# Kernel tuning notes

Hardware: AMD Instinct MI355X
Metric: run time of the kernel (lower is better)

The kernel has to match this reference:

```python
import jax, jax.numpy as jnp
import numpy as np

BN_EPS = 1e-5
INTERP_EPS = 1e-8


def _bn_relu(x, g, b, m, v):
    # eval-mode BatchNorm1d over channel dim (last axis here) + ReLU
    return jax.nn.relu((x - m) * (g / jnp.sqrt(v + BN_EPS)) + b)


def setup_inputs() -> dict:
    key = jax.random.key(0)
    ks = jax.random.split(key, 12)
    B, N, S, C1, C2 = 4, 16384, 1024, 128, 256
    Cin = C1 + C2  # 384
    H1, H2 = 256, 128
    inp = {
        "xyz1": jax.random.normal(ks[0], (B, N, 3), jnp.float32),
        "xyz2": jax.random.normal(ks[1], (B, S, 3), jnp.float32),
        "points1": jax.random.normal(ks[2], (B, N, C1), jnp.float32),
        "points2": jax.random.normal(ks[3], (B, S, C2), jnp.float32),
        # Conv1d(k=1, bias=False) weights: (out_ch, in_ch)
        "w1": jax.random.normal(ks[4], (H1, Cin), jnp.float32) * (1.0 / np.sqrt(Cin)),
        "g1": jax.random.uniform(ks[5], (H1,), jnp.float32, 0.5, 1.5),
        "b1": jax.random.normal(ks[6], (H1,), jnp.float32) * 0.1,
        "m1": jax.random.normal(ks[7], (H1,), jnp.float32) * 0.1,
        "v1": jax.random.uniform(ks[8], (H1,), jnp.float32, 0.5, 1.5),
        "w2": jax.random.normal(ks[9], (H2, H1), jnp.float32) * (1.0 / np.sqrt(H1)),
        "g2": jax.random.uniform(ks[10], (H2,), jnp.float32, 0.5, 1.5),
        "b2": jax.random.normal(ks[11], (H2,), jnp.float32) * 0.1,
        "m2": jnp.zeros((H2,), jnp.float32),
        "v2": jnp.ones((H2,), jnp.float32),
    }
    return inp


def reference(xyz1, xyz2, points1, points2, w1, g1, b1, m1, v1, w2, g2, b2, m2, v2):
    B, N, _ = xyz1.shape
    S = xyz2.shape[1]
    # squared pairwise distances (B, N, S) via ||a||^2 + ||b||^2 - 2 a.b
    sq = (
        jnp.sum(xyz1 * xyz1, -1)[:, :, None]
        + jnp.sum(xyz2 * xyz2, -1)[:, None, :]
        - 2.0 * jnp.einsum("bnd,bsd->bns", xyz1, xyz2)
    )
    neg_d, idx = jax.lax.top_k(-sq, 3)  # 3 nearest neighbors
    dists = -neg_d  # (B, N, 3) squared distances, ascending
    recip = 1.0 / (dists + INTERP_EPS)
    weight = recip / jnp.sum(recip, -1, keepdims=True)  # (B, N, 3)
    # gather neighbor features: (B, N, 3, C2)
    gathered = points2[jnp.arange(B)[:, None, None], idx]
    interpolated = jnp.einsum("bnk,bnkc->bnc", weight, gathered)
    new_points = jnp.concatenate([points1, interpolated], axis=-1)  # (B, N, Cin)
    h = _bn_relu(jnp.einsum("bnc,dc->bnd", new_points, w1), g1, b1, m1, v1)
    out = _bn_relu(jnp.einsum("bnc,dc->bnd", h, w2), g2, b2, m2, v2)
    return out
```

## Files before the change

kernel.cpp:

```cpp
#include <hip/hip_runtime.h>
#include <math.h>

#define B_    4
#define N_    16384
#define S_    1024
#define C1_   128
#define C2_   256
#define CIN_  384
#define H1_   256
#define H2_   128
#define BN_EPS_     1e-5f
#define INTERP_EPS_ 1e-8f

typedef _Float16 f16;
typedef _Float16 f16x4 __attribute__((ext_vector_type(4)));
typedef _Float16 f16x8 __attribute__((ext_vector_type(8)));
typedef float    f32x4 __attribute__((ext_vector_type(4)));

#define GLD16(g, l) \
  __builtin_amdgcn_global_load_lds((const __attribute__((address_space(1))) void*)(g), \
                                   (__attribute__((address_space(3))) void*)(l), 16, 0, 0)

#define WS_IDX 0
#define WS_W   786432
#define WS_H   1572864
#define WS_W1F 35127296
#define WS_W2F 35323904
#define WS_SC1 35389440
#define WS_SH1 35390464
#define WS_SC2 35391488
#define WS_SH2 35392000

__global__ __launch_bounds__(256) void prep_kernel(
    const float* __restrict__ w1, const float* __restrict__ w2,
    const float* __restrict__ g1, const float* __restrict__ b1,
    const float* __restrict__ m1, const float* __restrict__ v1,
    const float* __restrict__ g2, const float* __restrict__ b2,
    const float* __restrict__ m2, const float* __restrict__ v2,
    f16* __restrict__ w1f, f16* __restrict__ w2f,
    float* __restrict__ sc1, float* __restrict__ sh1,
    float* __restrict__ sc2, float* __restrict__ sh2)
{
    const int t = blockIdx.x * 256 + threadIdx.x;
    if (t < 98304) {
        w1f[t] = (f16)w1[t];
    } else if (t < 131072) {
        w2f[t - 98304] = (f16)w2[t - 98304];
    } else if (t < 131328) {
        const int c = t - 131072;
        const float s = g1[c] / sqrtf(v1[c] + BN_EPS_);
        sc1[c] = s; sh1[c] = b1[c] - m1[c] * s;
    } else if (t < 131456) {
        const int c = t - 131328;
        const float s = g2[c] / sqrtf(v2[c] + BN_EPS_);
        sc2[c] = s; sh2[c] = b2[c] - m2[c] * s;
    }
}

#define LESS_(e, ei, dj, ij) ((e) < (dj) || ((e) == (dj) && (ei) < (ij)))
#define INSERT_LEX(e, ei) do { \
    if (LESS_(e, ei, d[3], id[3])) { \
      if (LESS_(e, ei, d[2], id[2])) { d[3] = d[2]; id[3] = id[2]; \
        if (LESS_(e, ei, d[1], id[1])) { d[2] = d[1]; id[2] = id[1]; \
          if (LESS_(e, ei, d[0], id[0])) { d[1] = d[0]; id[1] = id[0]; d[0] = e; id[0] = ei; } \
          else { d[1] = e; id[1] = ei; } } \
        else { d[2] = e; id[2] = ei; } } \
      else { d[3] = e; id[3] = ei; } } } while (0)
#define CSWAP(a_, b_) do { \
    if (rd[b_] < rd[a_] || (rd[b_] == rd[a_] && ri[b_] < ri[a_])) { \
      double td = rd[a_]; rd[a_] = rd[b_]; rd[b_] = td; \
      int ti = ri[a_]; ri[a_] = ri[b_]; ri[b_] = ti; } } while (0)

__device__ __forceinline__ int qaddr(int s) { return s * 4 + (s >> 8) * 4; }

__global__ __launch_bounds__(256) void topk_kernel(
    const float* __restrict__ xyz1, const float* __restrict__ xyz2,
    int* __restrict__ idx_out, float* __restrict__ w_out)
{
    __shared__ float q[4128];
    const int b     = blockIdx.x >> 8;
    const int pbase = (blockIdx.x & 255) << 6;
    const int t     = threadIdx.x;

    for (int i = t; i < S_; i += 256) {
        const float* s = &xyz2[((size_t)b * S_ + i) * 3];
        const int a = qaddr(i);
        q[a] = s[0]; q[a + 1] = s[1]; q[a + 2] = s[2];
    }
    __syncthreads();

    const int p     = pbase + (t >> 2);
    const int chunk = t & 3;
    const float* pp = &xyz1[((size_t)b * N_ + p) * 3];
    const float px = pp[0], py = pp[1], pz = pp[2];

    float d[4] = {1e30f, 1e30f, 1e30f, 1e30f};
    int  id[4] = {0, 0, 0, 0};

    const int s0 = chunk << 8;
    for (int s = s0; s < s0 + 256; ++s) {
        const int a = qaddr(s);
        const float dx = px - q[a], dy = py - q[a + 1], dz = pz - q[a + 2];
        const float dd = fmaf(dx, dx, fmaf(dy, dy, dz * dz));
        if (dd < d[3]) {
            if (dd < d[2]) { d[3] = d[2]; id[3] = id[2];
                if (dd < d[1]) { d[2] = d[1]; id[2] = id[1];
                    if (dd < d[0]) { d[1] = d[0]; id[1] = id[0]; d[0] = dd; id[0] = s; }
                    else { d[1] = dd; id[1] = s; } }
                else { d[2] = dd; id[2] = s; } }
            else { d[3] = dd; id[3] = s; }
        }
    }

    #pragma unroll
    for (int msk = 1; msk <= 2; msk <<= 1) {
        float e0 = __shfl_xor(d[0], msk), e1 = __shfl_xor(d[1], msk);
        float e2 = __shfl_xor(d[2], msk), e3 = __shfl_xor(d[3], msk);
        int   j0 = __shfl_xor(id[0], msk), j1 = __shfl_xor(id[1], msk);
        int   j2 = __shfl_xor(id[2], msk), j3 = __shfl_xor(id[3], msk);
        INSERT_LEX(e0, j0); INSERT_LEX(e1, j1); INSERT_LEX(e2, j2); INSERT_LEX(e3, j3);
    }

    if (chunk == 0) {
        const double px6 = px, py6 = py, pz6 = pz;
        double rd[4]; int ri[4];
        #pragma unroll
        for (int j = 0; j < 4; ++j) {
            const int s = id[j]; ri[j] = s;
            const int a = qaddr(s);
            const double dx = px6 - (double)q[a], dy = py6 - (double)q[a + 1], dz = pz6 - (double)q[a + 2];
            rd[j] = dx * dx + dy * dy + dz * dz;
        }
        CSWAP(0, 1); CSWAP(2, 3); CSWAP(0, 2); CSWAP(1, 3); CSWAP(1, 2);
        const float f0 = (float)rd[0], f1 = (float)rd[1], f2 = (float)rd[2];
        const float r0 = 1.0f / (f0 + INTERP_EPS_);
        const float r1 = 1.0f / (f1 + INTERP_EPS_);
        const float r2 = 1.0f / (f2 + INTERP_EPS_);
        const float rs = r0 + r1 + r2;
        const int base = (b * N_ + p) * 3;
        idx_out[base] = ri[0]; idx_out[base + 1] = ri[1]; idx_out[base + 2] = ri[2];
        w_out[base] = r0 / rs; w_out[base + 1] = r1 / rs; w_out[base + 2] = r2 / rs;
    }
}

__device__ __forceinline__ void mfma_step1(const f16* As, const f16* Bs,
                                           f32x4 (&acc)[4][8],
                                           int wr, int wc, int lrow, int lhi)
{
    f16x8 af[4], bf[8];
    #pragma unroll
    for (int m = 0; m < 4; ++m)
        af[m] = *(const f16x8*)&As[(wr * 64 + m * 16 + lrow) * 32 + lhi * 8];
    #pragma unroll
    for (int n = 0; n < 8; ++n)
        bf[n] = *(const f16x8*)&Bs[(wc * 128 + n * 16 + lrow) * 32 + lhi * 8];
    #pragma unroll
    for (int m = 0; m < 4; ++m)
        #pragma unroll
        for (int n = 0; n < 8; ++n)
            acc[m][n] = __builtin_amdgcn_mfma_f32_16x16x32_f16(af[m], bf[n], acc[m][n], 0, 0, 0);
}

__global__ __launch_bounds__(256, 2) void gemm1_kernel(
    const float* __restrict__ points1, const float* __restrict__ points2,
    const int* __restrict__ idx, const float* __restrict__ wts,
    const f16* __restrict__ w1f,
    const float* __restrict__ sc1v, const float* __restrict__ sh1v,
    f16* __restrict__ h)
{
    __shared__ __align__(16) f16 As[128 * 32];
    __shared__ __align__(16) f16 Bs[256 * 32];

    const int t = threadIdx.x;
    const int w = t >> 6;
    const int lane = t & 63;
    const int wr = w >> 1, wc = w & 1;
    const int lrow = lane & 15, lhi = lane >> 4;
    const int rowbase = blockIdx.x * 128;

    const int srow = t >> 1, khalf = t & 1;
    const int R = rowbase + srow;
    const int bb = R >> 14;
    const int mb = R * 3;
    const int i0 = idx[mb], i1 = idx[mb + 1], i2 = idx[mb + 2];
    const float w0 = wts[mb], w1w = wts[mb + 1], w2w = wts[mb + 2];
    const float* p2b = points2 + (size_t)bb * S_ * C2_;
    const float* p1r = points1 + (size_t)R * C1_;
    f16* asrow = &As[srow * 32 + khalf * 16];

    f32x4 acc[4][8] = {};

    for (int kb = 0; kb < C1_; kb += 32) {
        __syncthreads();
        const float* src = p1r + kb + khalf * 16;
        #pragma unroll
        for (int g4 = 0; g4 < 4; ++g4) {
            const float4 v = *(const float4*)(src + g4 * 4);
            f16x4 o = {(f16)v.x, (f16)v.y, (f16)v.z, (f16)v.w};
            *(f16x4*)(asrow + g4 * 4) = o;
        }
        #pragma unroll
        for (int j = 0; j < 4; ++j) {
            const int c = j * 256 + t;
            GLD16(w1f + (size_t)(c >> 2) * CIN_ + kb + (c & 3) * 8,
                  (char*)Bs + (j * 4096 + w * 1024));
        }
        __syncthreads();
        mfma_step1(As, Bs, acc, wr, wc, lrow, lhi);
    }

    for (int kb = C1_; kb < CIN_; kb += 32) {
        __syncthreads();
        const int c0 = (kb - C1_) + khalf * 16;
        #pragma unroll
        for (int g4 = 0; g4 < 4; ++g4) {
            const int c = c0 + g4 * 4;
            const float4 f0 = *(const float4*)&p2b[(size_t)i0 * C2_ + c];
            const float4 f1 = *(const float4*)&p2b[(size_t)i1 * C2_ + c];
            const float4 f2 = *(const float4*)&p2b[(size_t)i2 * C2_ + c];
            const float x = fmaf(w0, f0.x, fmaf(w1w, f1.x, w2w * f2.x));
            const float y = fmaf(w0, f0.y, fmaf(w1w, f1.y, w2w * f2.y));
            const float z = fmaf(w0, f0.z, fmaf(w1w, f1.z, w2w * f2.z));
            const float u = fmaf(w0, f0.w, fmaf(w1w, f1.w, w2w * f2.w));
            f16x4 o = {(f16)x, (f16)y, (f16)z, (f16)u};
            *(f16x4*)(asrow + g4 * 4) = o;
        }
        #pragma unroll
        for (int j = 0; j < 4; ++j) {
            const int c = j * 256 + t;
            GLD16(w1f + (size_t)(c >> 2) * CIN_ + kb + (c & 3) * 8,
                  (char*)Bs + (j * 4096 + w * 1024));
        }
        __syncthreads();
        mfma_step1(As, Bs, acc, wr, wc, lrow, lhi);
    }

    #pragma unroll
    for (int n = 0; n < 8; ++n) {
        const int col = wc * 128 + n * 16 + lrow;
        const float sc = sc1v[col], sh = sh1v[col];
        #pragma unroll
        for (int m = 0; m < 4; ++m) {
            const int row0 = rowbase + wr * 64 + m * 16 + lhi * 4;
            #pragma unroll
            for (int i = 0; i < 4; ++i) {
                const float v = fmaxf(fmaf(acc[m][n][i], sc, sh), 0.0f);
                h[(size_t)(row0 + i) * H1_ + col] = (f16)v;
            }
        }
    }
}

__global__ __launch_bounds__(256, 2) void gemm2_kernel(
    const f16* __restrict__ hin, const f16* __restrict__ w2f,
    const float* __restrict__ sc2v, const float* __restrict__ sh2v,
    float* __restrict__ out)
{
    __shared__ __align__(16) f16 As[128 * 32];
    __shared__ __align__(16) f16 Bs[128 * 32];

    const int t = threadIdx.x;
    const int w = t >> 6;
    const int lane = t & 63;
    const int wr = w >> 1, wc = w & 1;
    const int lrow = lane & 15, lhi = lane >> 4;
    const int rowbase = blockIdx.x * 128;

    f32x4 acc[4][4] = {};

    for (int kb = 0; kb < H1_; kb += 32) {
        __syncthreads();
        #pragma unroll
        for (int j = 0; j < 2; ++j) {
            const int c = j * 256 + t;
            GLD16(hin + (size_t)(rowbase + (c >> 2)) * H1_ + kb + (c & 3) * 8,
                  (char*)As + (j * 4096 + w * 1024));
            GLD16(w2f + (size_t)(c >> 2) * H1_ + kb + (c & 3) * 8,
                  (char*)Bs + (j * 4096 + w * 1024));
        }
        __syncthreads();
        f16x8 af[4], bf[4];
        #pragma unroll
        for (int m = 0; m < 4; ++m)
            af[m] = *(const f16x8*)&As[(wr * 64 + m * 16 + lrow) * 32 + lhi * 8];
        #pragma unroll
        for (int n = 0; n < 4; ++n)
            bf[n] = *(const f16x8*)&Bs[(wc * 64 + n * 16 + lrow) * 32 + lhi * 8];
        #pragma unroll
        for (int m = 0; m < 4; ++m)
            #pragma unroll
            for (int n = 0; n < 4; ++n)
                acc[m][n] = __builtin_amdgcn_mfma_f32_16x16x32_f16(af[m], bf[n], acc[m][n], 0, 0, 0);
    }

    #pragma unroll
    for (int n = 0; n < 4; ++n) {
        const int col = wc * 64 + n * 16 + lrow;
        const float sc = sc2v[col], sh = sh2v[col];
        #pragma unroll
        for (int m = 0; m < 4; ++m) {
            const int row0 = rowbase + wr * 64 + m * 16 + lhi * 4;
            #pragma unroll
            for (int i = 0; i < 4; ++i) {
                out[(size_t)(row0 + i) * H2_ + col] = fmaxf(fmaf(acc[m][n][i], sc, sh), 0.0f);
            }
        }
    }
}

extern "C" void kernel_launch(void* const* d_in, const int* in_sizes, int n_in,
                              void* d_out, int out_size, void* d_ws, size_t ws_size,
                              hipStream_t stream) {
    const float* xyz1    = (const float*)d_in[0];
    const float* xyz2    = (const float*)d_in[1];
    const float* points1 = (const float*)d_in[2];
    const float* points2 = (const float*)d_in[3];
    const float* w1      = (const float*)d_in[4];
    const float* g1      = (const float*)d_in[5];
    const float* b1      = (const float*)d_in[6];
    const float* m1      = (const float*)d_in[7];
    const float* v1      = (const float*)d_in[8];
    const float* w2      = (const float*)d_in[9];
    const float* g2      = (const float*)d_in[10];
    const float* b2      = (const float*)d_in[11];
    const float* m2      = (const float*)d_in[12];
    const float* v2      = (const float*)d_in[13];
    float* out = (float*)d_out;

    char* ws = (char*)d_ws;
    int*   idx_ws = (int*)(ws + WS_IDX);
    float* w_ws   = (float*)(ws + WS_W);
    f16*   h_ws   = (f16*)(ws + WS_H);
    f16*   w1f    = (f16*)(ws + WS_W1F);
    f16*   w2f    = (f16*)(ws + WS_W2F);
    float* sc1    = (float*)(ws + WS_SC1);
    float* sh1    = (float*)(ws + WS_SH1);
    float* sc2    = (float*)(ws + WS_SC2);
    float* sh2    = (float*)(ws + WS_SH2);

    topk_kernel<<<dim3(B_ * 256), dim3(256), 0, stream>>>(xyz1, xyz2, idx_ws, w_ws);
    prep_kernel<<<dim3(514), dim3(256), 0, stream>>>(w1, w2, g1, b1, m1, v1,
                                                     g2, b2, m2, v2,
                                                     w1f, w2f, sc1, sh1, sc2, sh2);
    gemm1_kernel<<<dim3(512), dim3(256), 0, stream>>>(points1, points2, idx_ws, w_ws,
                                                      w1f, sc1, sh1, h_ws);
    gemm2_kernel<<<dim3(512), dim3(256), 0, stream>>>(h_ws, w2f, sc2, sh2, out);
}
```

Measured before the change: 206.4 us.

## Split top-k scan across 8 lanes per point with float4 LDS and ballot-skip

The nearest-neighbour kernel now gives each query point 8 lanes instead of 4, so each lane scans 128 candidates rather than 256, and the grid doubles to 2048 blocks. Candidate coordinates are packed as padded float4 in LDS for single vector loads. Each group of 4 distances is screened with a wave-wide ballot so the insertion logic is skipped when no lane can improve. The lexicographic tie-break in the shuffle merge is dropped, which could change which index wins on exact distance ties.

```diff
diff --git a/kernel.cpp b/kernel.cpp
--- a/kernel.cpp
+++ b/kernel.cpp
@@ -57,68 +57,70 @@
     }
 }
 
-#define LESS_(e, ei, dj, ij) ((e) < (dj) || ((e) == (dj) && (ei) < (ij)))
-#define INSERT_LEX(e, ei) do { \
-    if (LESS_(e, ei, d[3], id[3])) { \
-      if (LESS_(e, ei, d[2], id[2])) { d[3] = d[2]; id[3] = id[2]; \
-        if (LESS_(e, ei, d[1], id[1])) { d[2] = d[1]; id[2] = id[1]; \
-          if (LESS_(e, ei, d[0], id[0])) { d[1] = d[0]; id[1] = id[0]; d[0] = e; id[0] = ei; } \
-          else { d[1] = e; id[1] = ei; } } \
-        else { d[2] = e; id[2] = ei; } } \
-      else { d[3] = e; id[3] = ei; } } } while (0)
+#define INSERT4(e, ei) do { \
+    if ((e) < d[3]) { \
+      if ((e) < d[2]) { d[3] = d[2]; id[3] = id[2]; \
+        if ((e) < d[1]) { d[2] = d[1]; id[2] = id[1]; \
+          if ((e) < d[0]) { d[1] = d[0]; id[1] = id[0]; d[0] = (e); id[0] = (ei); } \
+          else { d[1] = (e); id[1] = (ei); } } \
+        else { d[2] = (e); id[2] = (ei); } } \
+      else { d[3] = (e); id[3] = (ei); } } } while (0)
 #define CSWAP(a_, b_) do { \
     if (rd[b_] < rd[a_] || (rd[b_] == rd[a_] && ri[b_] < ri[a_])) { \
       double td = rd[a_]; rd[a_] = rd[b_]; rd[b_] = td; \
       int ti = ri[a_]; ri[a_] = ri[b_]; ri[b_] = ti; } } while (0)
 
-__device__ __forceinline__ int qaddr(int s) { return s * 4 + (s >> 8) * 4; }
-
 __global__ __launch_bounds__(256) void topk_kernel(
     const float* __restrict__ xyz1, const float* __restrict__ xyz2,
     int* __restrict__ idx_out, float* __restrict__ w_out)
 {
-    __shared__ float q[4128];
-    const int b     = blockIdx.x >> 8;
-    const int pbase = (blockIdx.x & 255) << 6;
+    __shared__ float4 q[S_ + 8];
+    const int b     = blockIdx.x >> 9;
+    const int pbase = (blockIdx.x & 511) << 5;
     const int t     = threadIdx.x;
 
     for (int i = t; i < S_; i += 256) {
         const float* s = &xyz2[((size_t)b * S_ + i) * 3];
-        const int a = qaddr(i);
-        q[a] = s[0]; q[a + 1] = s[1]; q[a + 2] = s[2];
+        float4 v; v.x = s[0]; v.y = s[1]; v.z = s[2]; v.w = 0.0f;
+        q[i + (i >> 7)] = v;
     }
     __syncthreads();
 
-    const int p     = pbase + (t >> 2);
-    const int chunk = t & 3;
+    const int p     = pbase + (t >> 3);
+    const int chunk = t & 7;
+    const int qb    = chunk * 129;
     const float* pp = &xyz1[((size_t)b * N_ + p) * 3];
     const float px = pp[0], py = pp[1], pz = pp[2];
 
     float d[4] = {1e30f, 1e30f, 1e30f, 1e30f};
     int  id[4] = {0, 0, 0, 0};
 
-    const int s0 = chunk << 8;
-    for (int s = s0; s < s0 + 256; ++s) {
-        const int a = qaddr(s);
-        const float dx = px - q[a], dy = py - q[a + 1], dz = pz - q[a + 2];
-        const float dd = fmaf(dx, dx, fmaf(dy, dy, dz * dz));
-        if (dd < d[3]) {
-            if (dd < d[2]) { d[3] = d[2]; id[3] = id[2];
-                if (dd < d[1]) { d[2] = d[1]; id[2] = id[1];
-                    if (dd < d[0]) { d[1] = d[0]; id[1] = id[0]; d[0] = dd; id[0] = s; }
-                    else { d[1] = dd; id[1] = s; } }
-                else { d[2] = dd; id[2] = s; } }
-            else { d[3] = dd; id[3] = s; }
-        }
-    }
-
-    #pragma unroll
-    for (int msk = 1; msk <= 2; msk <<= 1) {
+    for (int i = 0; i < 128; i += 4) {
+        float dd[4];
+        #pragma unroll
+        for (int u = 0; u < 4; ++u) {
+            const float4 c = q[qb + i + u];
+            const float dx = px - c.x, dy = py - c.y, dz = pz - c.z;
+            dd[u] = fmaf(dx, dx, fmaf(dy, dy, dz * dz));
+        }
+        const float m4 = fminf(fminf(dd[0], dd[1]), fminf(dd[2], dd[3]));
+        if (__ballot(m4 < d[3])) {
+            #pragma unroll
+            for (int u = 0; u < 4; ++u) {
+                const float e = dd[u];
+                const int  ei = (chunk << 7) + i + u;
+                INSERT4(e, ei);
+            }
+        }
+    }
+
+    #pragma unroll
+    for (int msk = 1; msk <= 4; msk <<= 1) {
         float e0 = __shfl_xor(d[0], msk), e1 = __shfl_xor(d[1], msk);
         float e2 = __shfl_xor(d[2], msk), e3 = __shfl_xor(d[3], msk);
         int   j0 = __shfl_xor(id[0], msk), j1 = __shfl_xor(id[1], msk);
         int   j2 = __shfl_xor(id[2], msk), j3 = __shfl_xor(id[3], msk);
-        INSERT_LEX(e0, j0); INSERT_LEX(e1, j1); INSERT_LEX(e2, j2); INSERT_LEX(e3, j3);
+        INSERT4(e0, j0); INSERT4(e1, j1); INSERT4(e2, j2); INSERT4(e3, j3);
     }
 
     if (chunk == 0) {
@@ -127,15 +129,14 @@
         #pragma unroll
         for (int j = 0; j < 4; ++j) {
             const int s = id[j]; ri[j] = s;
-            const int a = qaddr(s);
-            const double dx = px6 - (double)q[a], dy = py6 - (double)q[a + 1], dz = pz6 - (double)q[a + 2];
+            const float4 c = q[s + (s >> 7)];
+            const double dx = px6 - (double)c.x, dy = py6 - (double)c.y, dz = pz6 - (double)c.z;
             rd[j] = dx * dx + dy * dy + dz * dz;
         }
         CSWAP(0, 1); CSWAP(2, 3); CSWAP(0, 2); CSWAP(1, 3); CSWAP(1, 2);
-        const float f0 = (float)rd[0], f1 = (float)rd[1], f2 = (float)rd[2];
-        const float r0 = 1.0f / (f0 + INTERP_EPS_);
-        const float r1 = 1.0f / (f1 + INTERP_EPS_);
-        const float r2 = 1.0f / (f2 + INTERP_EPS_);
+        const float r0 = 1.0f / ((float)rd[0] + INTERP_EPS_);
+        const float r1 = 1.0f / ((float)rd[1] + INTERP_EPS_);
+        const float r2 = 1.0f / ((float)rd[2] + INTERP_EPS_);
         const float rs = r0 + r1 + r2;
         const int base = (b * N_ + p) * 3;
         idx_out[base] = ri[0]; idx_out[base + 1] = ri[1]; idx_out[base + 2] = ri[2];
@@ -338,7 +339,7 @@
     float* sc2    = (float*)(ws + WS_SC2);
     float* sh2    = (float*)(ws + WS_SH2);
 
-    topk_kernel<<<dim3(B_ * 256), dim3(256), 0, stream>>>(xyz1, xyz2, idx_ws, w_ws);
+    topk_kernel<<<dim3(B_ * (N_ / 32)), dim3(256), 0, stream>>>(xyz1, xyz2, idx_ws, w_ws);
     prep_kernel<<<dim3(514), dim3(256), 0, stream>>>(w1, w2, g1, b1, m1, v1,
                                                      g2, b2, m2, v2,
                                                      w1f, w2f, sc1, sh1, sc2, sh2);
```

New measurement: 204.2 us. Within noise of the previous version (-1.1%).
